# Optimization experiments

Hardware: AMD Instinct MI355X
Metric: run time of the kernel (lower is better)

Reference implementation:

```python
import jax, jax.numpy as jnp
import numpy as np

# Architecture constants (match init_kwargs)
A = 4            # num_areas
E_PER = 512      # excitatory units per area
I_PER = 128      # inhibitory units per area
H = A * (E_PER + I_PER)   # 2560 hidden units, order: [all E (area-major), all I]
NUM_OBJS = 2
IN_UNITS = 64
IN = NUM_OBJS * IN_UNITS  # 128 input units
DT, TAU_X = 0.02, 0.1
ALPHA_X = DT / TAU_X


def _build_masks():
    """Signed Dale's-law connectivity masks, as in _get_connectivity_mask_* ."""
    # inter-area recurrent connectivity: nearest-neighbor hierarchy + self
    rec = np.eye(A) + np.eye(A, k=1) + np.eye(A, k=-1)
    ee = np.kron(rec, np.ones((E_PER, E_PER)))
    ei = np.kron(np.eye(A), np.ones((E_PER, I_PER)))   # E<-I only within area
    ie = np.kron(rec, np.ones((I_PER, E_PER)))
    ii = np.kron(np.eye(A), np.ones((I_PER, I_PER)))
    conn = np.block([[ee, ei], [ie, ii]])
    # sign mask: first e_size columns excitatory (+1), rest inhibitory (-1)
    sign = np.concatenate([np.ones(A * E_PER), -np.ones(A * I_PER)])[None, :]
    rec_mask = conn * sign
    np.fill_diagonal(rec_mask, 0.0)  # remove_diag=True in h2h EILinear
    # input mask: only area 0 receives external input; e_prop=1 for x2h (all +1)
    in_area = np.zeros((A, NUM_OBJS)); in_area[0, :] = 1.0
    in_e = np.kron(in_area, np.ones((E_PER, IN_UNITS)))
    in_i = np.kron(in_area, np.ones((I_PER, IN_UNITS)))
    in_mask = np.concatenate([in_e, in_i], axis=0)
    return jnp.asarray(rec_mask, jnp.float32), jnp.asarray(in_mask, jnp.float32)


def setup_inputs() -> dict:
    key = jax.random.key(0)
    k1, k2, k3 = jax.random.split(key, 3)
    T, B = 500, 64
    inputs = jax.random.normal(k1, (T, B, IN), dtype=jnp.float32)
    W_rec = jax.random.normal(k2, (H, H), dtype=jnp.float32) / np.sqrt(H)
    b_rec = jnp.zeros((H,), dtype=jnp.float32)
    W_in = jax.random.normal(k3, (H, IN), dtype=jnp.float32) / np.sqrt(IN)
    return {"inputs": inputs, "W_rec": W_rec, "b_rec": b_rec, "W_in": W_in}


def reference(inputs, W_rec, b_rec, W_in):
    rec_mask, in_mask = _build_masks()
    # EILinear effective weights: pos_func=abs, times signed connectivity mask
    W_rec_eff = jnp.abs(W_rec) * rec_mask          # [H, H]
    W_in_eff = jnp.abs(W_in) * in_mask             # [H, IN]
    # input projection for all timesteps at once
    proj = jnp.einsum('tbi,hi->tbh', inputs, W_in_eff)  # [T, B, H]

    def retanh(x):
        return jnp.tanh(jax.nn.relu(x))

    def step(carry, u_t):
        x, r = carry
        pre = r @ W_rec_eff.T + b_rec + u_t        # h2h(r) + x2h(u)
        x = (1.0 - ALPHA_X) * x + ALPHA_X * pre    # leaky integration
        r = retanh(x)
        return (x, r), r

    B = inputs.shape[1]
    x0 = jnp.zeros((B, H), dtype=inputs.dtype)     # x0 (train_init_state=False)
    (_, _), rates = jax.lax.scan(step, (x0, retanh(x0)), proj)
    return rates  # [T, B, H] firing rates
```

## Files before the change

kernel.cpp:

```cpp
#include <hip/hip_runtime.h>
#include <math.h>

#define Hn   2560
#define Bn   64
#define INW  128
#define ETOT 2048
#define HGn  160
#define MAXC 13
#define NBLK 160
#define MAXI 7

typedef __attribute__((ext_vector_type(8))) _Float16 half8;
typedef __attribute__((ext_vector_type(4))) float  floatx4;

__global__ void build_apack(const float* __restrict__ Wrec,
                            const float* __restrict__ Win,
                            _Float16* __restrict__ Af) {
  int hg = blockIdx.x, c = blockIdx.y;
  int a = (hg < 128) ? (hg >> 5) : ((hg - 128) >> 3);
  int nE = (a == 0 || a == 3) ? 8 : 12;
  int nch = nE + 1 + (a == 0 ? 1 : 0);
  if (c >= nch) return;
  int h0 = hg * 16;
  int tid = threadIdx.x;
  int kq = tid >> 6, L = tid & 63;
  int m = L & 15, q = L >> 4;
  int h = h0 + m;

  const float* src; int k0, stride; float sgn; bool isIn = false;
  if (c < nE)       { k0 = ((a == 0 ? 0 : a - 1) << 9) + (c << 7); src = Wrec; stride = Hn;  sgn =  1.f; }
  else if (c == nE) { k0 = ETOT + (a << 7);                        src = Wrec; stride = Hn;  sgn = -1.f; }
  else              { k0 = 0;                                      src = Win;  stride = INW; sgn =  1.f; isIn = true; }

  _Float16 hi8[8], lo8[8];
  #pragma unroll
  for (int j = 0; j < 8; ++j) {
    int k = k0 + kq * 32 + q * 8 + j;
    float w = fabsf(src[(size_t)h * stride + k]);
    if (!isIn && k == h) w = 0.f;
    w *= sgn;
    _Float16 wh = (_Float16)w;
    hi8[j] = wh;
    lo8[j] = (_Float16)(w - (float)wh);
  }
  _Float16* outp = Af + (size_t)(hg * MAXC + c) * 4096;
  *(uint4*)(outp + (kq * 2 + 0) * 512 + L * 8) = *(const uint4*)hi8;
  *(uint4*)(outp + (kq * 2 + 1) * 512 + L * 8) = *(const uint4*)lo8;
}

#define LOADI(B0,B1,B2,B3,P) \
  asm volatile("global_load_dwordx4 %0, %4, off sc0 sc1\n\t" \
               "global_load_dwordx4 %1, %4, off offset:1024 sc0 sc1\n\t" \
               "global_load_dwordx4 %2, %4, off offset:2048 sc0 sc1\n\t" \
               "global_load_dwordx4 %3, %4, off offset:3072 sc0 sc1" \
               : "=&v"(B0), "=&v"(B1), "=&v"(B2), "=&v"(B3) \
               : "v"(P) : "memory")

#define MFMA8(i, B0,B1,B2,B3) do { \
  ac0 = __builtin_amdgcn_mfma_f32_16x16x32_f16(ah[i], B0, ac0, 0, 0, 0); \
  ac0 = __builtin_amdgcn_mfma_f32_16x16x32_f16(al[i], B0, ac0, 0, 0, 0); \
  ac1 = __builtin_amdgcn_mfma_f32_16x16x32_f16(ah[i], B1, ac1, 0, 0, 0); \
  ac1 = __builtin_amdgcn_mfma_f32_16x16x32_f16(al[i], B1, ac1, 0, 0, 0); \
  ac2 = __builtin_amdgcn_mfma_f32_16x16x32_f16(ah[i], B2, ac2, 0, 0, 0); \
  ac2 = __builtin_amdgcn_mfma_f32_16x16x32_f16(al[i], B2, ac2, 0, 0, 0); \
  ac3 = __builtin_amdgcn_mfma_f32_16x16x32_f16(ah[i], B3, ac3, 0, 0, 0); \
  ac3 = __builtin_amdgcn_mfma_f32_16x16x32_f16(al[i], B3, ac3, 0, 0, 0); \
} while (0)

__global__ __launch_bounds__(512, 1) void rnn_persist(
    const _Float16* __restrict__ Af,
    const float* __restrict__ inputs,
    _Float16* __restrict__ rfA, _Float16* __restrict__ rfB,
    const float* __restrict__ brec,
    float* __restrict__ rates,
    unsigned* bar, int T)
{
  __shared__ float red[8][1056];
  __shared__ float rrt[16][68];
  __shared__ float bb[16];

  const int hg  = blockIdx.x;
  const int tid = threadIdx.x;
  const int w   = tid >> 6, L = tid & 63;
  const int h0  = hg * 16;
  const int a   = (hg < 128) ? (hg >> 5) : ((hg - 128) >> 3);
  const int nE  = (a == 0 || a == 3) ? 8 : 12;
  const int SK  = (nE + 1 + (a == 0 ? 1 : 0)) * 4;
  const int ktE0 = (a == 0 ? 0 : a - 1) * 16;
  const int ktI0 = 64 + a * 4;

  unsigned* bsub = bar + (hg & 7) * 64;
  unsigned* bmas = bar + 8 * 64;

  if (tid < 16) bb[tid] = brec[h0 + tid];

  half8 ah[MAXI], al[MAXI];
  int   boff[MAXI];
  bool  act[MAXI], isin[MAXI];
  const _Float16* Abase = Af + (size_t)hg * MAXC * 4096;
  #pragma unroll
  for (int i = 0; i < MAXI; ++i) {
    half8 zz = {0,0,0,0,0,0,0,0};
    ah[i] = zz; al[i] = zz;
    int ks = w + i * 8;
    act[i]  = ks < SK;
    isin[i] = false;
    boff[i] = 0;
    if (act[i]) {
      int c = ks >> 2, kq = ks & 3;
      const _Float16* Ap = Abase + (size_t)c * 4096 + (size_t)(kq * 2) * 512 + (size_t)L * 8;
      ah[i] = *(const half8*)Ap;
      al[i] = *(const half8*)(Ap + 512);
      if (c <= nE) {
        int kt = (c < nE) ? (ktE0 + c * 4 + kq) : (ktI0 + kq);
        boff[i] = kt * 2048 + L * 8;
      } else {
        isin[i] = true;
        boff[i] = kq * 32 + (L >> 4) * 8;
      }
    }
  }
  #pragma unroll
  for (int i = 0; i < MAXI; ++i)
    asm volatile("" : "+v"(ah[i]), "+v"(al[i]));

  float xv[2] = {0.f, 0.f};

  __syncthreads();

  for (int t = 0; t < T; ++t) {
    const _Float16* __restrict__ rs = (t & 1) ? rfB : rfA;
    _Float16* __restrict__ rd       = (t & 1) ? rfA : rfB;

    floatx4 ac0 = {0.f,0.f,0.f,0.f}, ac1 = {0.f,0.f,0.f,0.f};
    floatx4 ac2 = {0.f,0.f,0.f,0.f}, ac3 = {0.f,0.f,0.f,0.f};

    #pragma unroll
    for (int i = 0; i < MAXI; ++i) {
      if (act[i] && isin[i]) {
        const float* ip = inputs + (size_t)t * (Bn * INW) + boff[i];
        int nb = L & 15;
        half8 b0, b1, b2, b3;
        #pragma unroll
        for (int j = 0; j < 8; ++j) b0[j] = (_Float16)ip[(nb +  0) * INW + j];
        #pragma unroll
        for (int j = 0; j < 8; ++j) b1[j] = (_Float16)ip[(nb + 16) * INW + j];
        #pragma unroll
        for (int j = 0; j < 8; ++j) b2[j] = (_Float16)ip[(nb + 32) * INW + j];
        #pragma unroll
        for (int j = 0; j < 8; ++j) b3[j] = (_Float16)ip[(nb + 48) * INW + j];
        MFMA8(i, b0, b1, b2, b3);
      }
    }

    half8 Bv0[MAXI], Bv1[MAXI], Bv2[MAXI], Bv3[MAXI];
    #pragma unroll
    for (int i = 0; i < MAXI; ++i) {
      if (act[i] && !isin[i]) {
        const _Float16* p = rs + boff[i];
        LOADI(Bv0[i], Bv1[i], Bv2[i], Bv3[i], p);
      }
    }
    asm volatile("s_waitcnt vmcnt(0)" ::: "memory");
    __builtin_amdgcn_sched_barrier(0);

    #pragma unroll
    for (int i = 0; i < MAXI; ++i) {
      if (act[i] && !isin[i])
        MFMA8(i, Bv0[i], Bv1[i], Bv2[i], Bv3[i]);
    }

    #pragma unroll
    for (int p = 0; p < 4; ++p) {
      int m = (L >> 4) * 4 + p;
      float* rw = &red[w][m * 66 + (L & 15)];
      rw[ 0] = ac0[p];
      rw[16] = ac1[p];
      rw[32] = ac2[p];
      rw[48] = ac3[p];
    }
    __syncthreads();

    #pragma unroll
    for (int e = 0; e < 2; ++e) {
      int elem = tid + e * 512;
      int m = elem >> 6, n = elem & 63;
      float s = 0.f;
      #pragma unroll
      for (int j = 0; j < 8; ++j) s += red[j][m * 66 + n];
      float x = 0.8f * xv[e] + 0.2f * (s + bb[m]);
      xv[e] = x;
      rrt[m][n] = tanhf(fmaxf(x, 0.f));
    }
    __syncthreads();

    if (tid < 128) {
      int bt = tid >> 5, Lq = tid & 31;
      int Lp = (hg & 1) * 32 + Lq;
      half8 vv;
      #pragma unroll
      for (int j = 0; j < 8; ++j)
        vv[j] = (_Float16)rrt[(Lq >> 4) * 8 + j][bt * 16 + (Lq & 15)];
      _Float16* dst = rd + (size_t)((hg >> 1) * 4 + bt) * 512 + (size_t)Lp * 8;
      asm volatile("global_store_dwordx4 %0, %1, off sc0 sc1\n\t"
                   "s_waitcnt vmcnt(0)"
                   :: "v"(dst), "v"(vv) : "memory");
    }
    if (tid >= 256) {
      int tt = tid - 256;
      int b = tt >> 2, hq = tt & 3;
      floatx4 o;
      o.x = rrt[hq * 4 + 0][b];
      o.y = rrt[hq * 4 + 1][b];
      o.z = rrt[hq * 4 + 2][b];
      o.w = rrt[hq * 4 + 3][b];
      __builtin_nontemporal_store(o,
          (floatx4*)(rates + (size_t)t * (Bn * Hn) + (size_t)b * Hn + h0 + hq * 4));
    }
    __syncthreads();

    if (t + 1 < T) {
      if (tid == 0) {
        unsigned g = (unsigned)(t + 1);
        unsigned s = __hip_atomic_fetch_add(bsub, 1u, __ATOMIC_RELAXED,
                                            __HIP_MEMORY_SCOPE_AGENT);
        if (s == g * 20u - 1u)
          __hip_atomic_fetch_add(bmas, 1u, __ATOMIC_RELAXED,
                                 __HIP_MEMORY_SCOPE_AGENT);
        while (__hip_atomic_load(bmas, __ATOMIC_RELAXED,
                                 __HIP_MEMORY_SCOPE_AGENT) < g * 8u)
          __builtin_amdgcn_s_sleep(2);
      }
      __syncthreads();
    }
  }
}

extern "C" void kernel_launch(void* const* d_in, const int* in_sizes, int n_in,
                              void* d_out, int out_size, void* d_ws, size_t ws_size,
                              hipStream_t stream) {
  const float* inputs = (const float*)d_in[0];
  const float* Wrec   = (const float*)d_in[1];
  const float* brec   = (const float*)d_in[2];
  const float* Win    = (const float*)d_in[3];
  int T = in_sizes[0] / (Bn * INW);

  char* base = (char*)d_ws;
  size_t off = 0;
  _Float16* Af  = (_Float16*)(base + off); off += (size_t)HGn * MAXC * 4096 * 2;
  _Float16* rfA = (_Float16*)(base + off); off += (size_t)80 * 4 * 512 * 2;
  _Float16* rfB = (_Float16*)(base + off); off += (size_t)80 * 4 * 512 * 2;
  unsigned* bar = (unsigned*)(base + off); off += 4096;

  (void)hipMemsetAsync(rfA, 0, (size_t)80 * 4 * 512 * 2, stream);
  (void)hipMemsetAsync(bar, 0, 4096, stream);

  build_apack<<<dim3(HGn, MAXC), 256, 0, stream>>>(Wrec, Win, Af);

  float* rates = (float*)d_out;
  rnn_persist<<<NBLK, 512, 0, stream>>>(Af, inputs, rfA, rfB, brec, rates,
                                        bar, T);
}
```

Measured before the change: 3.217 ms.

## Flatten grid barrier, split-phase arrive, batch loads, fast tanh

Replaces the two-level grid barrier with a single flat counter. Each block now arrives before storing its rates output and waits only afterwards, so the output store overlaps the barrier. The recurrent-operand loads become fixed-size batched asm groups (4 plus 1–3) with embedded waits, replacing predicated per-slot loads with one wait. tanh is replaced with an exp2/rcp approximation, and launch bounds change to 2 blocks per SM. Risks include more contention on one atomic counter, less load overlap from splitting into two wait points, and a slight accuracy change from the tanh approximation.

```diff
diff --git a/kernel.cpp b/kernel.cpp
--- a/kernel.cpp
+++ b/kernel.cpp
@@ -48,11 +48,69 @@
   *(uint4*)(outp + (kq * 2 + 1) * 512 + L * 8) = *(const uint4*)lo8;
 }
 
-#define LOADI(B0,B1,B2,B3,P) \
+#define LOADQ(Q0,Q1,Q2,Q3,R0,R1,R2,R3,S0,S1,S2,S3,U0,U1,U2,U3,P0,P1,P2,P3) \
+  asm volatile("global_load_dwordx4 %0, %16, off sc0 sc1\n\t" \
+               "global_load_dwordx4 %1, %16, off offset:1024 sc0 sc1\n\t" \
+               "global_load_dwordx4 %2, %16, off offset:2048 sc0 sc1\n\t" \
+               "global_load_dwordx4 %3, %16, off offset:3072 sc0 sc1\n\t" \
+               "global_load_dwordx4 %4, %17, off sc0 sc1\n\t" \
+               "global_load_dwordx4 %5, %17, off offset:1024 sc0 sc1\n\t" \
+               "global_load_dwordx4 %6, %17, off offset:2048 sc0 sc1\n\t" \
+               "global_load_dwordx4 %7, %17, off offset:3072 sc0 sc1\n\t" \
+               "global_load_dwordx4 %8, %18, off sc0 sc1\n\t" \
+               "global_load_dwordx4 %9, %18, off offset:1024 sc0 sc1\n\t" \
+               "global_load_dwordx4 %10, %18, off offset:2048 sc0 sc1\n\t" \
+               "global_load_dwordx4 %11, %18, off offset:3072 sc0 sc1\n\t" \
+               "global_load_dwordx4 %12, %19, off sc0 sc1\n\t" \
+               "global_load_dwordx4 %13, %19, off offset:1024 sc0 sc1\n\t" \
+               "global_load_dwordx4 %14, %19, off offset:2048 sc0 sc1\n\t" \
+               "global_load_dwordx4 %15, %19, off offset:3072 sc0 sc1\n\t" \
+               "s_waitcnt vmcnt(0)" \
+               : "=&v"(Q0), "=&v"(Q1), "=&v"(Q2), "=&v"(Q3), \
+                 "=&v"(R0), "=&v"(R1), "=&v"(R2), "=&v"(R3), \
+                 "=&v"(S0), "=&v"(S1), "=&v"(S2), "=&v"(S3), \
+                 "=&v"(U0), "=&v"(U1), "=&v"(U2), "=&v"(U3) \
+               : "v"(P0), "v"(P1), "v"(P2), "v"(P3) : "memory")
+
+#define LOADT(Q0,Q1,Q2,Q3,R0,R1,R2,R3,S0,S1,S2,S3,P0,P1,P2) \
+  asm volatile("global_load_dwordx4 %0, %12, off sc0 sc1\n\t" \
+               "global_load_dwordx4 %1, %12, off offset:1024 sc0 sc1\n\t" \
+               "global_load_dwordx4 %2, %12, off offset:2048 sc0 sc1\n\t" \
+               "global_load_dwordx4 %3, %12, off offset:3072 sc0 sc1\n\t" \
+               "global_load_dwordx4 %4, %13, off sc0 sc1\n\t" \
+               "global_load_dwordx4 %5, %13, off offset:1024 sc0 sc1\n\t" \
+               "global_load_dwordx4 %6, %13, off offset:2048 sc0 sc1\n\t" \
+               "global_load_dwordx4 %7, %13, off offset:3072 sc0 sc1\n\t" \
+               "global_load_dwordx4 %8, %14, off sc0 sc1\n\t" \
+               "global_load_dwordx4 %9, %14, off offset:1024 sc0 sc1\n\t" \
+               "global_load_dwordx4 %10, %14, off offset:2048 sc0 sc1\n\t" \
+               "global_load_dwordx4 %11, %14, off offset:3072 sc0 sc1\n\t" \
+               "s_waitcnt vmcnt(0)" \
+               : "=&v"(Q0), "=&v"(Q1), "=&v"(Q2), "=&v"(Q3), \
+                 "=&v"(R0), "=&v"(R1), "=&v"(R2), "=&v"(R3), \
+                 "=&v"(S0), "=&v"(S1), "=&v"(S2), "=&v"(S3) \
+               : "v"(P0), "v"(P1), "v"(P2) : "memory")
+
+#define LOAD8(X0,X1,X2,X3,Y0,Y1,Y2,Y3,PA,PB) \
+  asm volatile("global_load_dwordx4 %0, %8, off sc0 sc1\n\t" \
+               "global_load_dwordx4 %1, %8, off offset:1024 sc0 sc1\n\t" \
+               "global_load_dwordx4 %2, %8, off offset:2048 sc0 sc1\n\t" \
+               "global_load_dwordx4 %3, %8, off offset:3072 sc0 sc1\n\t" \
+               "global_load_dwordx4 %4, %9, off sc0 sc1\n\t" \
+               "global_load_dwordx4 %5, %9, off offset:1024 sc0 sc1\n\t" \
+               "global_load_dwordx4 %6, %9, off offset:2048 sc0 sc1\n\t" \
+               "global_load_dwordx4 %7, %9, off offset:3072 sc0 sc1\n\t" \
+               "s_waitcnt vmcnt(0)" \
+               : "=&v"(X0), "=&v"(X1), "=&v"(X2), "=&v"(X3), \
+                 "=&v"(Y0), "=&v"(Y1), "=&v"(Y2), "=&v"(Y3) \
+               : "v"(PA), "v"(PB) : "memory")
+
+#define LOAD4(B0,B1,B2,B3,P) \
   asm volatile("global_load_dwordx4 %0, %4, off sc0 sc1\n\t" \
                "global_load_dwordx4 %1, %4, off offset:1024 sc0 sc1\n\t" \
                "global_load_dwordx4 %2, %4, off offset:2048 sc0 sc1\n\t" \
-               "global_load_dwordx4 %3, %4, off offset:3072 sc0 sc1" \
+               "global_load_dwordx4 %3, %4, off offset:3072 sc0 sc1\n\t" \
+               "s_waitcnt vmcnt(0)" \
                : "=&v"(B0), "=&v"(B1), "=&v"(B2), "=&v"(B3) \
                : "v"(P) : "memory")
 
@@ -67,7 +125,7 @@
   ac3 = __builtin_amdgcn_mfma_f32_16x16x32_f16(al[i], B3, ac3, 0, 0, 0); \
 } while (0)
 
-__global__ __launch_bounds__(512, 1) void rnn_persist(
+__global__ __launch_bounds__(512, 2) void rnn_persist(
     const _Float16* __restrict__ Af,
     const float* __restrict__ inputs,
     _Float16* __restrict__ rfA, _Float16* __restrict__ rfB,
@@ -88,9 +146,6 @@
   const int SK  = (nE + 1 + (a == 0 ? 1 : 0)) * 4;
   const int ktE0 = (a == 0 ? 0 : a - 1) * 16;
   const int ktI0 = 64 + a * 4;
-
-  unsigned* bsub = bar + (hg & 7) * 64;
-  unsigned* bmas = bar + 8 * 64;
 
   if (tid < 16) bb[tid] = brec[h0 + tid];
 
@@ -124,6 +179,11 @@
   for (int i = 0; i < MAXI; ++i)
     asm volatile("" : "+v"(ah[i]), "+v"(al[i]));
 
+  int Rn = 0;
+  while (Rn < MAXI && act[Rn] && !isin[Rn]) ++Rn;
+  const bool hasIn = (Rn < MAXI) && act[Rn] && isin[Rn];
+  const int  rem   = Rn - 4;
+
   float xv[2] = {0.f, 0.f};
 
   __syncthreads();
@@ -135,39 +195,54 @@
     floatx4 ac0 = {0.f,0.f,0.f,0.f}, ac1 = {0.f,0.f,0.f,0.f};
     floatx4 ac2 = {0.f,0.f,0.f,0.f}, ac3 = {0.f,0.f,0.f,0.f};
 
-    #pragma unroll
-    for (int i = 0; i < MAXI; ++i) {
-      if (act[i] && isin[i]) {
-        const float* ip = inputs + (size_t)t * (Bn * INW) + boff[i];
-        int nb = L & 15;
-        half8 b0, b1, b2, b3;
-        #pragma unroll
-        for (int j = 0; j < 8; ++j) b0[j] = (_Float16)ip[(nb +  0) * INW + j];
-        #pragma unroll
-        for (int j = 0; j < 8; ++j) b1[j] = (_Float16)ip[(nb + 16) * INW + j];
-        #pragma unroll
-        for (int j = 0; j < 8; ++j) b2[j] = (_Float16)ip[(nb + 32) * INW + j];
-        #pragma unroll
-        for (int j = 0; j < 8; ++j) b3[j] = (_Float16)ip[(nb + 48) * INW + j];
-        MFMA8(i, b0, b1, b2, b3);
-      }
-    }
-
-    half8 Bv0[MAXI], Bv1[MAXI], Bv2[MAXI], Bv3[MAXI];
-    #pragma unroll
-    for (int i = 0; i < MAXI; ++i) {
-      if (act[i] && !isin[i]) {
-        const _Float16* p = rs + boff[i];
-        LOADI(Bv0[i], Bv1[i], Bv2[i], Bv3[i], p);
-      }
-    }
-    asm volatile("s_waitcnt vmcnt(0)" ::: "memory");
-    __builtin_amdgcn_sched_barrier(0);
-
-    #pragma unroll
-    for (int i = 0; i < MAXI; ++i) {
-      if (act[i] && !isin[i])
-        MFMA8(i, Bv0[i], Bv1[i], Bv2[i], Bv3[i]);
+    if (hasIn) {
+      const float* ip = inputs + (size_t)t * (Bn * INW) + boff[Rn];
+      int nb = L & 15;
+      half8 b0, b1, b2, b3;
+      #pragma unroll
+      for (int j = 0; j < 8; ++j) b0[j] = (_Float16)ip[(nb +  0) * INW + j];
+      #pragma unroll
+      for (int j = 0; j < 8; ++j) b1[j] = (_Float16)ip[(nb + 16) * INW + j];
+      #pragma unroll
+      for (int j = 0; j < 8; ++j) b2[j] = (_Float16)ip[(nb + 32) * INW + j];
+      #pragma unroll
+      for (int j = 0; j < 8; ++j) b3[j] = (_Float16)ip[(nb + 48) * INW + j];
+      MFMA8(Rn, b0, b1, b2, b3);
+    }
+
+    {
+      half8 q0,q1,q2,q3, r0,r1,r2,r3, s0,s1,s2,s3, u0,u1,u2,u3;
+      const _Float16* p0 = rs + boff[0];
+      const _Float16* p1 = rs + boff[1];
+      const _Float16* p2 = rs + boff[2];
+      const _Float16* p3 = rs + boff[3];
+      LOADQ(q0,q1,q2,q3, r0,r1,r2,r3, s0,s1,s2,s3, u0,u1,u2,u3, p0,p1,p2,p3);
+      MFMA8(0, q0,q1,q2,q3);
+      MFMA8(1, r0,r1,r2,r3);
+      MFMA8(2, s0,s1,s2,s3);
+      MFMA8(3, u0,u1,u2,u3);
+    }
+    if (rem == 3) {
+      half8 q0,q1,q2,q3, r0,r1,r2,r3, s0,s1,s2,s3;
+      const _Float16* p0 = rs + boff[4];
+      const _Float16* p1 = rs + boff[5];
+      const _Float16* p2 = rs + boff[6];
+      LOADT(q0,q1,q2,q3, r0,r1,r2,r3, s0,s1,s2,s3, p0,p1,p2);
+      MFMA8(4, q0,q1,q2,q3);
+      MFMA8(5, r0,r1,r2,r3);
+      MFMA8(6, s0,s1,s2,s3);
+    } else if (rem == 2) {
+      half8 q0,q1,q2,q3, r0,r1,r2,r3;
+      const _Float16* p0 = rs + boff[4];
+      const _Float16* p1 = rs + boff[5];
+      LOAD8(q0,q1,q2,q3, r0,r1,r2,r3, p0,p1);
+      MFMA8(4, q0,q1,q2,q3);
+      MFMA8(5, r0,r1,r2,r3);
+    } else if (rem == 1) {
+      half8 q0,q1,q2,q3;
+      const _Float16* p0 = rs + boff[4];
+      LOAD4(q0,q1,q2,q3, p0);
+      MFMA8(4, q0,q1,q2,q3);
     }
 
     #pragma unroll
@@ -190,7 +265,9 @@
       for (int j = 0; j < 8; ++j) s += red[j][m * 66 + n];
       float x = 0.8f * xv[e] + 0.2f * (s + bb[m]);
       xv[e] = x;
-      rrt[m][n] = tanhf(fmaxf(x, 0.f));
+      float xr = fmaxf(x, 0.f);
+      float e2 = __builtin_amdgcn_exp2f(xr * 2.885390081777926814f);
+      rrt[m][n] = 1.0f - 2.0f * __builtin_amdgcn_rcpf(e2 + 1.0f);
     }
     __syncthreads();
 
@@ -206,6 +283,13 @@
                    "s_waitcnt vmcnt(0)"
                    :: "v"(dst), "v"(vv) : "memory");
     }
+    __syncthreads();
+
+    unsigned g = (unsigned)(t + 1);
+    if (t + 1 < T && tid == 0)
+      __hip_atomic_fetch_add(bar, 1u, __ATOMIC_RELAXED,
+                             __HIP_MEMORY_SCOPE_AGENT);
+
     if (tid >= 256) {
       int tt = tid - 256;
       int b = tt >> 2, hq = tt & 3;
@@ -217,19 +301,12 @@
       __builtin_nontemporal_store(o,
           (floatx4*)(rates + (size_t)t * (Bn * Hn) + (size_t)b * Hn + h0 + hq * 4));
     }
-    __syncthreads();
 
     if (t + 1 < T) {
       if (tid == 0) {
-        unsigned g = (unsigned)(t + 1);
-        unsigned s = __hip_atomic_fetch_add(bsub, 1u, __ATOMIC_RELAXED,
-                                            __HIP_MEMORY_SCOPE_AGENT);
-        if (s == g * 20u - 1u)
-          __hip_atomic_fetch_add(bmas, 1u, __ATOMIC_RELAXED,
-                                 __HIP_MEMORY_SCOPE_AGENT);
-        while (__hip_atomic_load(bmas, __ATOMIC_RELAXED,
-                                 __HIP_MEMORY_SCOPE_AGENT) < g * 8u)
-          __builtin_amdgcn_s_sleep(2);
+        while (__hip_atomic_load(bar, __ATOMIC_RELAXED,
+                                 __HIP_MEMORY_SCOPE_AGENT) < g * (unsigned)NBLK)
+          __builtin_amdgcn_s_sleep(1);
       }
       __syncthreads();
     }
```

Measured after the change: 5.684 ms. 1.77x slower.
